# Kernel tuning notes

Measured on AMD Instinct MI355X. Metric: run time of the kernel, lower is better.

## Reference

```python
import jax, jax.numpy as jnp
import numpy as np

B, S, D = 16, 1024, 768
H = 12
HD = D // H  # 64


def setup_inputs() -> dict:
    key = jax.random.key(0)
    k1, k2, k3 = jax.random.split(key, 3)
    scale_in = 1.0 / np.sqrt(D)
    return {
        "x": jax.random.normal(k1, (B, S, D), dtype=jnp.float32),
        "w_qkv": jax.random.normal(k2, (3 * D, D), dtype=jnp.float32) * scale_in,
        "b_qkv": jnp.zeros((3 * D,), dtype=jnp.float32),
        "w_proj": jax.random.normal(k3, (D, D), dtype=jnp.float32) * scale_in,
        "b_proj": jnp.zeros((D,), dtype=jnp.float32),
    }


def reference(x, w_qkv, b_qkv, w_proj, b_proj):
    b, s, d = x.shape
    scale = HD ** -0.5
    # qkv projection: [B,S,3D] -> [3,B,H,S,HD]
    qkv = x @ w_qkv.T + b_qkv
    qkv = qkv.reshape(b, s, 3, H, HD).transpose(2, 0, 3, 1, 4)
    q, k, v = qkv[0], qkv[1], qkv[2]
    q = q * scale
    attn = jnp.einsum("bhqd,bhkd->bhqk", q, k)  # [B,H,S,S]
    attn = jax.nn.softmax(attn, axis=-1)
    # attn_dropout is identity in eval mode
    z = jnp.einsum("bhqk,bhkd->bhqd", attn, v)
    z = z.transpose(0, 2, 1, 3).reshape(b, s, d)
    return z @ w_proj.T + b_proj
```

## Files before the change

kernel.cpp:

```cpp
#include <hip/hip_runtime.h>
#include <hip/hip_bf16.h>
#include <cstdint>
#include <cstddef>

typedef __attribute__((ext_vector_type(8))) short short8;
typedef __attribute__((ext_vector_type(4))) float floatx4;
typedef __attribute__((ext_vector_type(16))) float floatx16;
typedef unsigned short u16;

__device__ __forceinline__ u16 f2bf(float f) {
  unsigned u = __float_as_uint(f);
  u += 0x7FFFu + ((u >> 16) & 1u);
  return (u16)(u >> 16);
}

__device__ __forceinline__ unsigned cvt_pk_bf16(float a, float b) {
  unsigned r;
  asm("v_cvt_pk_bf16_f32 %0, %1, %2" : "=v"(r) : "v"(a), "v"(b));
  return r;
}

__device__ __forceinline__ float fexp2(float x) {
#if __has_builtin(__builtin_amdgcn_exp2f)
  return __builtin_amdgcn_exp2f(x);
#else
  float r;
  asm("v_exp_f32 %0, %1\n\ts_nop 1" : "=v"(r) : "v"(x));
  return r;
#endif
}

__device__ __forceinline__ float frcp(float x) {
#if __has_builtin(__builtin_amdgcn_rcpf)
  return __builtin_amdgcn_rcpf(x);
#else
  float r;
  asm("v_rcp_f32 %0, %1\n\ts_nop 1" : "=v"(r) : "v"(x));
  return r;
#endif
}

__device__ __forceinline__ void gload16(const u16* g, u16* l) {
  __builtin_amdgcn_global_load_lds(
      (const __attribute__((address_space(1))) void*)g,
      (__attribute__((address_space(3))) void*)l, 16, 0, 0);
}

__device__ __forceinline__ void phase_barrier() {
  __builtin_amdgcn_sched_barrier(0);
  __builtin_amdgcn_s_barrier();
  __builtin_amdgcn_sched_barrier(0);
}

__global__ void cvt3_kernel(const float* __restrict__ a, u16* __restrict__ oa, int na4,
                            const float* __restrict__ b, u16* __restrict__ ob, int nb4,
                            const float* __restrict__ c, u16* __restrict__ oc, int nc4) {
  int i = blockIdx.x * blockDim.x + threadIdx.x;
  int stride = gridDim.x * blockDim.x;
  int ntot = na4 + nb4 + nc4;
  for (int idx = i; idx < ntot; idx += stride) {
    const float* src; u16* dst; int j = idx;
    if (j < na4)            { src = a; dst = oa; }
    else if (j < na4 + nb4) { src = b; dst = ob; j -= na4; }
    else                    { src = c; dst = oc; j -= na4 + nb4; }
    float4 v = reinterpret_cast<const float4*>(src)[j];
    ushort4 o = make_ushort4(f2bf(v.x), f2bf(v.y), f2bf(v.z), f2bf(v.w));
    reinterpret_cast<ushort4*>(dst)[j] = o;
  }
}

template<bool OUTF32>
__global__ __launch_bounds__(512) void gemm_bt256p(
    const u16* __restrict__ A, const u16* __restrict__ B,
    const float* __restrict__ bias, void* __restrict__ Cout,
    int M, int N, int K, int qcols, float qscale)
{
  __shared__ u16 As[3 * 8192];
  __shared__ u16 Bs[3 * 8192];
  const int tid = threadIdx.x;
  const int lane = tid & 63, w = tid >> 6;
  const int l15 = lane & 15, lhi = lane >> 4;
  const int wm = w >> 2, wn = w & 3;

  const int mblocks = M >> 8;
  const int nb = N >> 8;
  const int bid = blockIdx.x;
  const int xcd = bid & 7;
  const int local = bid >> 3;
  const int mpx = mblocks >> 3;
  const int m0 = (xcd * mpx + local / nb) << 8;
  const int n0 = (local % nb) << 8;

  const int srow = tid >> 2;
  const int scol = (tid & 3) * 8;
  const u16* aptr = A + (size_t)(m0 + srow) * K + scol;
  const u16* bptr = B + (size_t)(n0 + srow) * K + scol;
  const size_t r128 = (size_t)128 * K;
  const int wbase = w * 512;
  const int ksteps = K >> 5;

  floatx4 acc[8][4] = {};

  gload16(aptr,             As + wbase);
  gload16(aptr + r128,      As + 4096 + wbase);
  gload16(bptr,             Bs + wbase);
  gload16(bptr + r128,      Bs + 4096 + wbase);
  gload16(aptr + 32,        As + 8192 + wbase);
  gload16(aptr + 32 + r128, As + 8192 + 4096 + wbase);
  gload16(bptr + 32,        Bs + 8192 + wbase);
  gload16(bptr + 32 + r128, Bs + 8192 + 4096 + wbase);
  asm volatile("s_waitcnt vmcnt(4)" ::: "memory");
  phase_barrier();

  const int rA = wm * 128 + l15;
  const int rB = wn * 64 + l15;
  const int kof = lhi * 8;

  int bc = 0, bs = 2;
  for (int t = 0; t < ksteps; ++t) {
    const bool stage = (t + 2 < ksteps);
    const int k2 = (t + 2) << 5;
    const u16* Ab = As + bc * 8192;
    const u16* Bb = Bs + bc * 8192;
    u16* Asd = As + bs * 8192 + wbase;
    u16* Bsd = Bs + bs * 8192 + wbase;
    short8 af[8], bf[4];

    if (stage) gload16(aptr + k2, Asd);
#pragma unroll
    for (int i = 0; i < 4; ++i)
      af[i] = *reinterpret_cast<const short8*>(&Ab[(rA + i * 16) * 32 + kof]);
    bf[0] = *reinterpret_cast<const short8*>(&Bb[(rB)      * 32 + kof]);
    bf[1] = *reinterpret_cast<const short8*>(&Bb[(rB + 16) * 32 + kof]);
    phase_barrier();
    __builtin_amdgcn_s_setprio(1);
#pragma unroll
    for (int i = 0; i < 4; ++i) {
      acc[i][0] = __builtin_amdgcn_mfma_f32_16x16x32_bf16(af[i], bf[0], acc[i][0], 0, 0, 0);
      acc[i][1] = __builtin_amdgcn_mfma_f32_16x16x32_bf16(af[i], bf[1], acc[i][1], 0, 0, 0);
    }
    __builtin_amdgcn_s_setprio(0);

    if (stage) gload16(aptr + k2 + r128, Asd + 4096);
    bf[2] = *reinterpret_cast<const short8*>(&Bb[(rB + 32) * 32 + kof]);
    bf[3] = *reinterpret_cast<const short8*>(&Bb[(rB + 48) * 32 + kof]);
    phase_barrier();
    __builtin_amdgcn_s_setprio(1);
#pragma unroll
    for (int i = 0; i < 4; ++i) {
      acc[i][2] = __builtin_amdgcn_mfma_f32_16x16x32_bf16(af[i], bf[2], acc[i][2], 0, 0, 0);
      acc[i][3] = __builtin_amdgcn_mfma_f32_16x16x32_bf16(af[i], bf[3], acc[i][3], 0, 0, 0);
    }
    __builtin_amdgcn_s_setprio(0);

    if (stage) gload16(bptr + k2, Bsd);
#pragma unroll
    for (int i = 0; i < 4; ++i)
      af[4 + i] = *reinterpret_cast<const short8*>(&Ab[(rA + 64 + i * 16) * 32 + kof]);
    phase_barrier();
    __builtin_amdgcn_s_setprio(1);
#pragma unroll
    for (int i = 0; i < 4; ++i) {
      acc[4 + i][0] = __builtin_amdgcn_mfma_f32_16x16x32_bf16(af[4 + i], bf[0], acc[4 + i][0], 0, 0, 0);
      acc[4 + i][1] = __builtin_amdgcn_mfma_f32_16x16x32_bf16(af[4 + i], bf[1], acc[4 + i][1], 0, 0, 0);
    }
    __builtin_amdgcn_s_setprio(0);

    if (stage) gload16(bptr + k2 + r128, Bsd + 4096);
    phase_barrier();
    __builtin_amdgcn_s_setprio(1);
#pragma unroll
    for (int i = 0; i < 4; ++i) {
      acc[4 + i][2] = __builtin_amdgcn_mfma_f32_16x16x32_bf16(af[4 + i], bf[2], acc[4 + i][2], 0, 0, 0);
      acc[4 + i][3] = __builtin_amdgcn_mfma_f32_16x16x32_bf16(af[4 + i], bf[3], acc[4 + i][3], 0, 0, 0);
    }
    __builtin_amdgcn_s_setprio(0);

    if (t + 1 < ksteps) {
      if (stage) asm volatile("s_waitcnt vmcnt(4)" ::: "memory");
      else       asm volatile("s_waitcnt vmcnt(0)" ::: "memory");
      phase_barrier();
    }
    bc = (bc == 2) ? 0 : bc + 1;
    bs = (bs == 2) ? 0 : bs + 1;
  }

#pragma unroll
  for (int i = 0; i < 8; ++i)
#pragma unroll
    for (int j = 0; j < 4; ++j) {
      int row = m0 + wm * 128 + i * 16 + lhi * 4;
      int col = n0 + wn * 64 + j * 16 + l15;
      float bv = bias[col];
      float sc = (col < qcols) ? qscale : 1.0f;
#pragma unroll
      for (int r = 0; r < 4; ++r) {
        float v = (acc[i][j][r] + bv) * sc;
        if (OUTF32) reinterpret_cast<float*>(Cout)[(size_t)(row + r) * N + col] = v;
        else        reinterpret_cast<u16*>(Cout)[(size_t)(row + r) * N + col] = f2bf(v);
      }
    }
}

__global__ __launch_bounds__(256) void vtrans_kernel(
    const u16* __restrict__ qkv, u16* __restrict__ vt)
{
  __shared__ u16 T[64][72];
  const int idx = blockIdx.x;
  const int st = idx & 15;
  const int bh = idx >> 4;
  const int b = bh / 12, h = bh % 12;
  const int t = threadIdx.x;
  const int r2 = t >> 3, c8 = (t & 7) * 8;

  const u16* src = qkv + ((size_t)(b * 1024 + st * 64)) * 2304 + 1536 + h * 64;
#pragma unroll
  for (int rr = 0; rr < 2; ++rr) {
    int s = rr * 32 + r2;
    short8 v = *reinterpret_cast<const short8*>(src + (size_t)s * 2304 + c8);
    *reinterpret_cast<short8*>(&T[s][c8]) = v;
  }
  __syncthreads();
  u16* dst = vt + (size_t)bh * 64 * 1024 + st * 64;
#pragma unroll
  for (int rr = 0; rr < 2; ++rr) {
    int d = rr * 32 + r2;
    short8 o;
#pragma unroll
    for (int j = 0; j < 8; ++j) o[j] = T[c8 + j][d];
    *reinterpret_cast<short8*>(dst + (size_t)d * 1024 + c8) = o;
  }
}

__global__ __launch_bounds__(512) void attn9_kernel(
    const u16* __restrict__ qkv, const u16* __restrict__ vt, u16* __restrict__ z)
{
  constexpr int LDK = 72;
  constexpr int SLOT = 64 * LDK;
  __shared__ u16 Ks[2 * SLOT];
  __shared__ u16 Vs[2 * SLOT];

  const int tid = threadIdx.x;
  const int lane = tid & 63, w = tid >> 6;
  const int l31 = lane & 31, hi = lane >> 5;

  const int idx = blockIdx.x;
  const int head = idx % 192;
  const int qt   = idx / 192;
  const int b = head / 12, h = head % 12;

  const size_t rowbase = (size_t)b * 1024;
  const u16* Qp  = qkv + rowbase * 2304 + h * 64;
  const u16* Kp  = Qp + 768;
  const u16* Vtp = vt + (size_t)head * 64 * 1024;

  const int q0 = qt * 256 + w * 32;

  short8 qf[4];
#pragma unroll
  for (int c = 0; c < 4; ++c)
    qf[c] = *reinterpret_cast<const short8*>(
        Qp + (size_t)(q0 + l31) * 2304 + c * 16 + hi * 8);

  union { unsigned u[4]; short8 v; } ONE;
#pragma unroll
  for (int i = 0; i < 4; ++i) ONE.u[i] = 0x3F803F80u;
  const short8 ones = ONE.v;

  const int srow = tid >> 3, scol = (tid & 7) * 8;

  const u16* kstage = Kp + (size_t)srow * 2304 + scol;
  const u16* vstage = Vtp + (size_t)srow * 1024 + scol;
  constexpr size_t KADV = (size_t)64 * 2304;
  constexpr size_t VADV = 64;

  u16* const ksw = &Ks[srow * LDK + scol];
  u16* const vsw = &Vs[srow * LDK + scol];
  const u16* const ks0 = &Ks[l31 * LDK + hi * 8];
  const u16* const vs0 = &Vs[l31 * LDK + hi * 8];

  short8 kvr = *reinterpret_cast<const short8*>(kstage);
  short8 vvr = *reinterpret_cast<const short8*>(vstage);
  kstage += KADV; vstage += VADV;

  floatx16 oacc0 = {}, oacc1 = {}, lacc = {};

  for (int kt = 0; kt < 16; ++kt) {
    const int so = (kt & 1) * SLOT;
    *reinterpret_cast<short8*>(ksw + so) = kvr;
    *reinterpret_cast<short8*>(vsw + so) = vvr;
    __syncthreads();

    if (kt < 15) {
      kvr = *reinterpret_cast<const short8*>(kstage);
      vvr = *reinterpret_cast<const short8*>(vstage);
      kstage += KADV; vstage += VADV;
    }

    const u16* ka = ks0 + so;
    const u16* va = vs0 + so;

    floatx16 s0 = {}, s1 = {};
    __builtin_amdgcn_s_setprio(1);
#pragma unroll
    for (int c = 0; c < 4; ++c) {
      short8 kf0 = *reinterpret_cast<const short8*>(ka + c * 16);
      short8 kf1 = *reinterpret_cast<const short8*>(ka + 32 * LDK + c * 16);
      s0 = __builtin_amdgcn_mfma_f32_32x32x16_bf16(kf0, qf[c], s0, 0, 0, 0);
      s1 = __builtin_amdgcn_mfma_f32_32x32x16_bf16(kf1, qf[c], s1, 0, 0, 0);
    }
    __builtin_amdgcn_s_setprio(0);

#pragma unroll
    for (int r = 0; r < 16; ++r) {
      s0[r] = fexp2(s0[r]);
      s1[r] = fexp2(s1[r]);
    }

    short8 pa[4];
#pragma unroll
    for (int c = 0; c < 4; ++c) {
      const floatx16& sv = (c >> 1) ? s1 : s0;
      const int B0 = (c & 1) * 8, B1 = B0 + 4;
      unsigned x0 = cvt_pk_bf16(sv[B0],     sv[B0 + 1]);
      unsigned x1 = cvt_pk_bf16(sv[B0 + 2], sv[B0 + 3]);
      unsigned y0 = cvt_pk_bf16(sv[B1],     sv[B1 + 1]);
      unsigned y1 = cvt_pk_bf16(sv[B1 + 2], sv[B1 + 3]);
      asm("s_nop 1\n\tv_permlane32_swap_b32 %0, %1" : "+v"(x0), "+v"(y0));
      asm("s_nop 1\n\tv_permlane32_swap_b32 %0, %1" : "+v"(x1), "+v"(y1));
      union { unsigned u[4]; short8 v; } P;
      P.u[0] = x0; P.u[1] = x1; P.u[2] = y0; P.u[3] = y1;
      pa[c] = P.v;
    }

    __builtin_amdgcn_s_setprio(1);
#pragma unroll
    for (int c = 0; c < 4; ++c) {
      short8 vf0 = *reinterpret_cast<const short8*>(va + c * 16);
      short8 vf1 = *reinterpret_cast<const short8*>(va + 32 * LDK + c * 16);
      oacc0 = __builtin_amdgcn_mfma_f32_32x32x16_bf16(pa[c], vf0, oacc0, 0, 0, 0);
      oacc1 = __builtin_amdgcn_mfma_f32_32x32x16_bf16(pa[c], vf1, oacc1, 0, 0, 0);
      lacc  = __builtin_amdgcn_mfma_f32_32x32x16_bf16(pa[c], ones, lacc, 0, 0, 0);
    }
    __builtin_amdgcn_s_setprio(0);
  }

#pragma unroll
  for (int r = 0; r < 16; ++r) {
    int q = (r & 3) + 8 * (r >> 2) + 4 * hi;
    float li = frcp(lacc[r]);
    size_t orow = (rowbase + q0 + q) * (size_t)768 + h * 64;
    z[orow + l31]      = f2bf(oacc0[r] * li);
    z[orow + 32 + l31] = f2bf(oacc1[r] * li);
  }
}

extern "C" void kernel_launch(void* const* d_in, const int* in_sizes, int n_in,
                              void* d_out, int out_size, void* d_ws, size_t ws_size,
                              hipStream_t stream) {
  (void)in_sizes; (void)n_in; (void)out_size; (void)ws_size;
  const float* x      = (const float*)d_in[0];
  const float* w_qkv  = (const float*)d_in[1];
  const float* b_qkv  = (const float*)d_in[2];
  const float* w_proj = (const float*)d_in[3];
  const float* b_proj = (const float*)d_in[4];
  float* out = (float*)d_out;

  const int BS = 16 * 1024;
  const int D = 768, N3 = 2304;
  const float QSC = 0.180336880f;

  u16* xb  = (u16*)d_ws;
  u16* wqb = xb  + (size_t)BS * D;
  u16* wpb = wqb + (size_t)N3 * D;
  u16* qkv = wpb + (size_t)D * D;
  u16* zb  = qkv + (size_t)BS * N3;
  u16* vtb = xb;

  cvt3_kernel<<<2048, 256, 0, stream>>>(x, xb, BS * D / 4,
                                        w_qkv, wqb, N3 * D / 4,
                                        w_proj, wpb, D * D / 4);

  gemm_bt256p<false><<<(BS / 256) * (N3 / 256), 512, 0, stream>>>(
      xb, wqb, b_qkv, qkv, BS, N3, D, 768, QSC);
  vtrans_kernel<<<192 * 16, 256, 0, stream>>>(qkv, vtb);
  attn9_kernel<<<192 * 4, 512, 0, stream>>>(qkv, vtb, zb);
  gemm_bt256p<true><<<(BS / 256) * (D / 256), 512, 0, stream>>>(
      zb, wpb, b_proj, out, BS, D, D, 0, 1.0f);
}
```

Baseline: 244.8 us.

## Restructure GEMM main loop to K=64 steps with XOR-swizzled LDS and staggered staging

```diff
diff --git a/kernel.cpp b/kernel.cpp
--- a/kernel.cpp
+++ b/kernel.cpp
@@ -51,6 +51,8 @@
   __builtin_amdgcn_s_barrier();
   __builtin_amdgcn_sched_barrier(0);
 }
+
+#define MFMA16(a, b, c) __builtin_amdgcn_mfma_f32_16x16x32_bf16((a), (b), (c), 0, 0, 0)
 
 __global__ void cvt3_kernel(const float* __restrict__ a, u16* __restrict__ oa, int na4,
                             const float* __restrict__ b, u16* __restrict__ ob, int nb4,
@@ -70,13 +72,13 @@
 }
 
 template<bool OUTF32>
-__global__ __launch_bounds__(512) void gemm_bt256p(
+__global__ __launch_bounds__(512) void gemm_bt256_8p(
     const u16* __restrict__ A, const u16* __restrict__ B,
     const float* __restrict__ bias, void* __restrict__ Cout,
     int M, int N, int K, int qcols, float qscale)
 {
-  __shared__ u16 As[3 * 8192];
-  __shared__ u16 Bs[3 * 8192];
+  __shared__ u16 As[4 * 8192];
+  __shared__ u16 Bs[4 * 8192];
   const int tid = threadIdx.x;
   const int lane = tid & 63, w = tid >> 6;
   const int l15 = lane & 15, lhi = lane >> 4;
@@ -91,99 +93,119 @@
   const int m0 = (xcd * mpx + local / nb) << 8;
   const int n0 = (local % nb) << 8;
 
-  const int srow = tid >> 2;
-  const int scol = (tid & 3) * 8;
-  const u16* aptr = A + (size_t)(m0 + srow) * K + scol;
-  const u16* bptr = B + (size_t)(n0 + srow) * K + scol;
-  const size_t r128 = (size_t)128 * K;
-  const int wbase = w * 512;
-  const int ksteps = K >> 5;
+  const int trow = tid >> 3;
+  const int cg8 = ((tid & 7) ^ ((tid >> 4) & 7)) * 8;
+  const u16* aS = A + (size_t)(m0 + trow) * K + cg8;
+  const u16* bS = B + (size_t)(n0 + trow) * K + cg8;
+  const int ksteps = K >> 6;
+
+  const int x7 = (l15 >> 1) & 7;
+  const int ko0 = l15 * 64 + (lhi ^ x7) * 8;
+  const int ko1 = l15 * 64 + ((4 + lhi) ^ x7) * 8;
+  const int brow = (wn & 1) * 64;
 
   floatx4 acc[8][4] = {};
 
-  gload16(aptr,             As + wbase);
-  gload16(aptr + r128,      As + 4096 + wbase);
-  gload16(bptr,             Bs + wbase);
-  gload16(bptr + r128,      Bs + 4096 + wbase);
-  gload16(aptr + 32,        As + 8192 + wbase);
-  gload16(aptr + 32 + r128, As + 8192 + 4096 + wbase);
-  gload16(bptr + 32,        Bs + 8192 + wbase);
-  gload16(bptr + 32 + r128, Bs + 8192 + 4096 + wbase);
-  asm volatile("s_waitcnt vmcnt(4)" ::: "memory");
+#define STG(matS, lds, v, h) do { \
+    gload16((matS) + (size_t)((h) * 128) * K + (size_t)(v) * 64, \
+            (lds) + ((((v) & 1) * 2 + (h)) * 8192) + w * 512); \
+    gload16((matS) + (size_t)((h) * 128 + 64) * K + (size_t)(v) * 64, \
+            (lds) + ((((v) & 1) * 2 + (h)) * 8192) + 4096 + w * 512); \
+  } while (0)
+
+  STG(aS, As, 0, 0); STG(aS, As, 0, 1);
+  STG(bS, Bs, 0, 0); STG(bS, Bs, 0, 1);
+  if (ksteps > 1) {
+    STG(bS, Bs, 1, 0); STG(bS, Bs, 1, 1);
+    asm volatile("s_waitcnt vmcnt(4)" ::: "memory");
+  } else {
+    asm volatile("s_waitcnt vmcnt(0)" ::: "memory");
+  }
   phase_barrier();
 
-  const int rA = wm * 128 + l15;
-  const int rB = wn * 64 + l15;
-  const int kof = lhi * 8;
-
-  int bc = 0, bs = 2;
-  for (int t = 0; t < ksteps; ++t) {
-    const bool stage = (t + 2 < ksteps);
-    const int k2 = (t + 2) << 5;
-    const u16* Ab = As + bc * 8192;
-    const u16* Bb = Bs + bc * 8192;
-    u16* Asd = As + bs * 8192 + wbase;
-    u16* Bsd = Bs + bs * 8192 + wbase;
-    short8 af[8], bf[4];
-
-    if (stage) gload16(aptr + k2, Asd);
+  for (int u = 0; u < ksteps; ++u) {
+    const int so = (u & 1) * 16384;
+    const u16* Ab = As + so + wm * 8192;
+    const u16* Bb = Bs + so + (wn >> 1) * 8192;
+    short8 af[4][2], bf[4][2];
+
+#pragma unroll
+    for (int i = 0; i < 4; ++i) {
+      af[i][0] = *reinterpret_cast<const short8*>(Ab + (i * 16) * 64 + ko0);
+      af[i][1] = *reinterpret_cast<const short8*>(Ab + (i * 16) * 64 + ko1);
+    }
+#pragma unroll
+    for (int j = 0; j < 2; ++j) {
+      bf[j][0] = *reinterpret_cast<const short8*>(Bb + (brow + j * 16) * 64 + ko0);
+      bf[j][1] = *reinterpret_cast<const short8*>(Bb + (brow + j * 16) * 64 + ko1);
+    }
+    if (u + 1 < ksteps) STG(aS, As, u + 1, 0);
+    phase_barrier();
+    __builtin_amdgcn_s_setprio(1);
 #pragma unroll
     for (int i = 0; i < 4; ++i)
-      af[i] = *reinterpret_cast<const short8*>(&Ab[(rA + i * 16) * 32 + kof]);
-    bf[0] = *reinterpret_cast<const short8*>(&Bb[(rB)      * 32 + kof]);
-    bf[1] = *reinterpret_cast<const short8*>(&Bb[(rB + 16) * 32 + kof]);
-    phase_barrier();
-    __builtin_amdgcn_s_setprio(1);
+#pragma unroll
+      for (int j = 0; j < 2; ++j) {
+        acc[i][j] = MFMA16(af[i][0], bf[j][0], acc[i][j]);
+        acc[i][j] = MFMA16(af[i][1], bf[j][1], acc[i][j]);
+      }
+    __builtin_amdgcn_s_setprio(0);
+    phase_barrier();
+
+#pragma unroll
+    for (int j = 2; j < 4; ++j) {
+      bf[j][0] = *reinterpret_cast<const short8*>(Bb + (brow + 32 + (j - 2) * 16) * 64 + ko0);
+      bf[j][1] = *reinterpret_cast<const short8*>(Bb + (brow + 32 + (j - 2) * 16) * 64 + ko1);
+    }
+    if (u + 1 < ksteps) STG(aS, As, u + 1, 1);
+    phase_barrier();
+    __builtin_amdgcn_s_setprio(1);
+#pragma unroll
+    for (int i = 0; i < 4; ++i)
+#pragma unroll
+      for (int j = 2; j < 4; ++j) {
+        acc[i][j] = MFMA16(af[i][0], bf[j][0], acc[i][j]);
+        acc[i][j] = MFMA16(af[i][1], bf[j][1], acc[i][j]);
+      }
+    __builtin_amdgcn_s_setprio(0);
+    phase_barrier();
+
 #pragma unroll
     for (int i = 0; i < 4; ++i) {
-      acc[i][0] = __builtin_amdgcn_mfma_f32_16x16x32_bf16(af[i], bf[0], acc[i][0], 0, 0, 0);
-      acc[i][1] = __builtin_amdgcn_mfma_f32_16x16x32_bf16(af[i], bf[1], acc[i][1], 0, 0, 0);
-    }
-    __builtin_amdgcn_s_setprio(0);
-
-    if (stage) gload16(aptr + k2 + r128, Asd + 4096);
-    bf[2] = *reinterpret_cast<const short8*>(&Bb[(rB + 32) * 32 + kof]);
-    bf[3] = *reinterpret_cast<const short8*>(&Bb[(rB + 48) * 32 + kof]);
-    phase_barrier();
-    __builtin_amdgcn_s_setprio(1);
-#pragma unroll
-    for (int i = 0; i < 4; ++i) {
-      acc[i][2] = __builtin_amdgcn_mfma_f32_16x16x32_bf16(af[i], bf[2], acc[i][2], 0, 0, 0);
-      acc[i][3] = __builtin_amdgcn_mfma_f32_16x16x32_bf16(af[i], bf[3], acc[i][3], 0, 0, 0);
-    }
-    __builtin_amdgcn_s_setprio(0);
-
-    if (stage) gload16(bptr + k2, Bsd);
+      af[i][0] = *reinterpret_cast<const short8*>(Ab + (64 + i * 16) * 64 + ko0);
+      af[i][1] = *reinterpret_cast<const short8*>(Ab + (64 + i * 16) * 64 + ko1);
+    }
+    if (u + 2 < ksteps) STG(bS, Bs, u + 2, 0);
+    phase_barrier();
+    __builtin_amdgcn_s_setprio(1);
 #pragma unroll
     for (int i = 0; i < 4; ++i)
-      af[4 + i] = *reinterpret_cast<const short8*>(&Ab[(rA + 64 + i * 16) * 32 + kof]);
-    phase_barrier();
-    __builtin_amdgcn_s_setprio(1);
-#pragma unroll
-    for (int i = 0; i < 4; ++i) {
-      acc[4 + i][0] = __builtin_amdgcn_mfma_f32_16x16x32_bf16(af[4 + i], bf[0], acc[4 + i][0], 0, 0, 0);
-      acc[4 + i][1] = __builtin_amdgcn_mfma_f32_16x16x32_bf16(af[4 + i], bf[1], acc[4 + i][1], 0, 0, 0);
-    }
-    __builtin_amdgcn_s_setprio(0);
-
-    if (stage) gload16(bptr + k2 + r128, Bsd + 4096);
-    phase_barrier();
-    __builtin_amdgcn_s_setprio(1);
-#pragma unroll
-    for (int i = 0; i < 4; ++i) {
-      acc[4 + i][2] = __builtin_amdgcn_mfma_f32_16x16x32_bf16(af[4 + i], bf[2], acc[4 + i][2], 0, 0, 0);
-      acc[4 + i][3] = __builtin_amdgcn_mfma_f32_16x16x32_bf16(af[4 + i], bf[3], acc[4 + i][3], 0, 0, 0);
-    }
-    __builtin_amdgcn_s_setprio(0);
-
-    if (t + 1 < ksteps) {
-      if (stage) asm volatile("s_waitcnt vmcnt(4)" ::: "memory");
-      else       asm volatile("s_waitcnt vmcnt(0)" ::: "memory");
-      phase_barrier();
-    }
-    bc = (bc == 2) ? 0 : bc + 1;
-    bs = (bs == 2) ? 0 : bs + 1;
-  }
+#pragma unroll
+      for (int j = 0; j < 2; ++j) {
+        acc[4 + i][j] = MFMA16(af[i][0], bf[j][0], acc[4 + i][j]);
+        acc[4 + i][j] = MFMA16(af[i][1], bf[j][1], acc[4 + i][j]);
+      }
+    __builtin_amdgcn_s_setprio(0);
+    phase_barrier();
+
+    if (u + 2 < ksteps) STG(bS, Bs, u + 2, 1);
+    phase_barrier();
+    __builtin_amdgcn_s_setprio(1);
+#pragma unroll
+    for (int i = 0; i < 4; ++i)
+#pragma unroll
+      for (int j = 2; j < 4; ++j) {
+        acc[4 + i][j] = MFMA16(af[i][0], bf[j][0], acc[4 + i][j]);
+        acc[4 + i][j] = MFMA16(af[i][1], bf[j][1], acc[4 + i][j]);
+      }
+    __builtin_amdgcn_s_setprio(0);
+    if (u + 1 < ksteps) {
+      if (u + 2 < ksteps) asm volatile("s_waitcnt vmcnt(4)" ::: "memory");
+      else                asm volatile("s_waitcnt vmcnt(0)" ::: "memory");
+    }
+    phase_barrier();
+  }
+#undef STG
 
 #pragma unroll
   for (int i = 0; i < 8; ++i)
@@ -381,10 +403,10 @@
                                         w_qkv, wqb, N3 * D / 4,
                                         w_proj, wpb, D * D / 4);
 
-  gemm_bt256p<false><<<(BS / 256) * (N3 / 256), 512, 0, stream>>>(
+  gemm_bt256_8p<false><<<(BS / 256) * (N3 / 256), 512, 0, stream>>>(
       xb, wqb, b_qkv, qkv, BS, N3, D, 768, QSC);
   vtrans_kernel<<<192 * 16, 256, 0, stream>>>(qkv, vtb);
   attn9_kernel<<<192 * 4, 512, 0, stream>>>(qkv, vtb, zb);
-  gemm_bt256p<true><<<(BS / 256) * (D / 256), 512, 0, stream>>>(
+  gemm_bt256_8p<true><<<(BS / 256) * (D / 256), 512, 0, stream>>>(
       zb, wpb, b_proj, out, BS, D, D, 0, 1.0f);
 }
```

Result: faster. 208.9 us, median of 4 (-14.6%).
